# Optimization experiments

Measured on AMD Instinct MI355X. Metric: run time of the kernel, lower is better.

## Reference

```python
import jax, jax.numpy as jnp
import numpy as np

T, B, D_IN, NQ = 256, 2048, 128, 8  # time, batch, input_dim, n_qubits == hidden_dim


def setup_inputs() -> dict:
    key = jax.random.key(0)
    ks = jax.random.split(key, 13)
    s = 1.0 / np.sqrt(D_IN + NQ)
    def lin(ka, kb):
        W = jax.random.uniform(ka, (D_IN + NQ, NQ), jnp.float32, -s, s)
        b = jax.random.uniform(kb, (NQ,), jnp.float32, -s, s)
        return W, b
    Wf, bf = lin(ks[0], ks[1])
    Wi, bi = lin(ks[2], ks[3])
    Wg, bg = lin(ks[4], ks[5])
    Wo, bo = lin(ks[6], ks[7])
    # trainable RX angles per wire for each of the 4 quantum gates
    thf = jax.random.normal(ks[8], (NQ,), jnp.float32) * 0.1
    thi = jax.random.normal(ks[9], (NQ,), jnp.float32) * 0.1
    thg = jax.random.normal(ks[10], (NQ,), jnp.float32) * 0.1
    tho = jax.random.normal(ks[11], (NQ,), jnp.float32) * 0.1
    inputs = jax.random.normal(ks[12], (T, B, D_IN), jnp.float32)
    return {"inputs": inputs, "Wf": Wf, "bf": bf, "Wi": Wi, "bi": bi,
            "Wg": Wg, "bg": bg, "Wo": Wo, "bo": bo,
            "thf": thf, "thi": thi, "thg": thg, "tho": tho}


def _qgate(lin_out, theta):
    # |0..0> -> RX(x_i) encode -> RX(theta_i) trainable -> <PauliZ_i> = cos(x_i + theta_i)
    return jnp.cos(lin_out + theta)


def reference(inputs, Wf, bf, Wi, bi, Wg, bg, Wo, bo, thf, thi, thg, tho):
    Bsz = inputs.shape[1]
    h0 = jnp.zeros((Bsz, NQ), inputs.dtype)
    c0 = jnp.zeros((Bsz, NQ), inputs.dtype)

    def step(carry, x):
        hx, cx = carry
        comb = jnp.concatenate([x, hx], axis=1)  # [B, D_IN+NQ]
        f = jax.nn.sigmoid(_qgate(comb @ Wf + bf, thf))
        i = jax.nn.sigmoid(_qgate(comb @ Wi + bi, thi))
        g = jnp.tanh(_qgate(comb @ Wg + bg, thg))
        o = jax.nn.sigmoid(_qgate(comb @ Wo + bo, tho))
        cx = f * cx + i * g
        hx = o * jnp.tanh(cx)
        return (hx, cx), hx

    (hx, cx), outputs = jax.lax.scan(step, (h0, c0), inputs)
    return outputs, hx, cx
```

## Files before the change

### kernel.cpp

```cpp
#include <hip/hip_runtime.h>

#define T_DIM 256
#define B_DIM 2048
#define D_IN_DIM 128
#define NQ 8
#define ROWS_PER_BLK 64
#define XSTRIDE 129
#define TSTRIDE 33

__global__ __launch_bounds__(256) void qlstm_gemm(
    const float* __restrict__ X,
    const float* __restrict__ Wf, const float* __restrict__ Wi,
    const float* __restrict__ Wg, const float* __restrict__ Wo,
    const float* __restrict__ bf, const float* __restrict__ bi,
    const float* __restrict__ bg, const float* __restrict__ bo,
    const float* __restrict__ thf, const float* __restrict__ thi,
    const float* __restrict__ thg, const float* __restrict__ tho,
    float4* __restrict__ Z)
{
    __shared__ float xs[ROWS_PER_BLK * XSTRIDE];

    const int t = (int)threadIdx.x;
    const int r0 = (int)blockIdx.x * ROWS_PER_BLK;

    const float4* Xg = (const float4*)(X + (size_t)r0 * D_IN_DIM);
#pragma unroll
    for (int i = 0; i < 8; i++) {
        int L = t + i * 256;
        float4 v = Xg[L];
        int row = L >> 5;
        int k4  = L & 31;
        float* d = &xs[row * XSTRIDE + k4 * 4];
        d[0] = v.x; d[1] = v.y; d[2] = v.z; d[3] = v.w;
    }
    __syncthreads();

    const int wid  = __builtin_amdgcn_readfirstlane(t >> 6);
    const int lane = t & 63;

    const float* W  = (wid == 0) ? Wf  : (wid == 1) ? Wi  : (wid == 2) ? Wg  : Wo;
    const float* BB = (wid == 0) ? bf  : (wid == 1) ? bi  : (wid == 2) ? bg  : bo;
    const float* TH = (wid == 0) ? thf : (wid == 1) ? thi : (wid == 2) ? thg : tho;

    float acc[NQ];
#pragma unroll
    for (int q = 0; q < NQ; q++) acc[q] = BB[q] + TH[q];

    const float* xrow = &xs[lane * XSTRIDE];
#pragma unroll 4
    for (int k = 0; k < D_IN_DIM; k++) {
        float xk = xrow[k];
#pragma unroll
        for (int q = 0; q < NQ; q++)
            acc[q] += xk * W[k * NQ + q];
    }

    __syncthreads();
    float* tile = xs;
#pragma unroll
    for (int q = 0; q < NQ; q++)
        tile[lane * TSTRIDE + q * 4 + wid] = acc[q];
    __syncthreads();

    float4* Zblk = Z + (size_t)r0 * NQ;
#pragma unroll
    for (int i = 0; i < 2; i++) {
        int F = t + i * 256;
        int r = F >> 3, q = F & 7;
        const float* s = &tile[r * TSTRIDE + q * 4];
        Zblk[F] = make_float4(s[0], s[1], s[2], s[3]);
    }
}

#define INV_2PI 0.15915494309189535f
#define L2E     1.4426950408889634f

__device__ __forceinline__ float hw_cos(float x) {
    return __builtin_amdgcn_cosf(x * INV_2PI);
}
__device__ __forceinline__ float hw_sig(float x) {
    return __builtin_amdgcn_rcpf(1.0f + __builtin_amdgcn_exp2f(-L2E * x));
}
__device__ __forceinline__ float hw_tanh(float x) {
    return 1.0f - 2.0f * __builtin_amdgcn_rcpf(__builtin_amdgcn_exp2f((2.0f * L2E) * x) + 1.0f);
}

#define BCAST8(x, J) \
    __int_as_float(__builtin_amdgcn_ds_swizzle(__float_as_int(x), ((J) << 5) | 0x18))

#define DOT_TERM(J) { \
    float hj = BCAST8(h, J); \
    accf += hj * whf[J]; acci += hj * whi[J]; \
    accg += hj * whg[J]; acco += hj * who[J]; }

#define LSTM_STEP(zv, outp) { \
    float accf = (zv).x, acci = (zv).y, accg = (zv).z, acco = (zv).w; \
    DOT_TERM(0) DOT_TERM(1) DOT_TERM(2) DOT_TERM(3) \
    DOT_TERM(4) DOT_TERM(5) DOT_TERM(6) DOT_TERM(7) \
    float fg = hw_sig(hw_cos(accf)); \
    float ig = hw_sig(hw_cos(acci)); \
    float gg = hw_tanh(hw_cos(accg)); \
    float og = hw_sig(hw_cos(acco)); \
    c = fg * c + ig * gg; \
    h = og * hw_tanh(c); \
    *(outp) = h; }

__global__ __launch_bounds__(64) void qlstm_recur(
    const float4* __restrict__ Z,
    const float* __restrict__ Wf, const float* __restrict__ Wi,
    const float* __restrict__ Wg, const float* __restrict__ Wo,
    float* __restrict__ out,
    float* __restrict__ state,
    int t0, int ct, int first, int last)
{
    const int tid = (int)blockIdx.x * 64 + (int)threadIdx.x;
    const int q   = tid & 7;

    float whf[8], whi[8], whg[8], who[8];
#pragma unroll
    for (int j = 0; j < 8; j++) {
        whf[j] = Wf[(D_IN_DIM + j) * NQ + q];
        whi[j] = Wi[(D_IN_DIM + j) * NQ + q];
        whg[j] = Wg[(D_IN_DIM + j) * NQ + q];
        who[j] = Wo[(D_IN_DIM + j) * NQ + q];
    }

    float h, c;
    if (first) { h = 0.0f; c = 0.0f; }
    else       { h = state[tid]; c = state[B_DIM * NQ + tid]; }

    const size_t stepsz = (size_t)B_DIM * NQ;
    const float4* Zp = Z + tid;
    float* outp = out + (size_t)t0 * stepsz + tid;

    float4 bufA[8], bufB[8];
#pragma unroll
    for (int s = 0; s < 8; s++) bufA[s] = Zp[(size_t)s * stepsz];

    for (int tb = 0; tb < ct; tb += 16) {
#pragma unroll
        for (int s = 0; s < 8; s++) bufB[s] = Zp[(size_t)(tb + 8 + s) * stepsz];
        __builtin_amdgcn_sched_barrier(0);
#pragma unroll
        for (int s = 0; s < 8; s++) {
            float4 z = bufA[s];
            LSTM_STEP(z, outp)
            outp += stepsz;
        }
        if (tb + 16 < ct) {
#pragma unroll
            for (int s = 0; s < 8; s++) bufA[s] = Zp[(size_t)(tb + 16 + s) * stepsz];
        }
        __builtin_amdgcn_sched_barrier(0);
#pragma unroll
        for (int s = 0; s < 8; s++) {
            float4 z = bufB[s];
            LSTM_STEP(z, outp)
            outp += stepsz;
        }
    }

    if (last) {
        out[(size_t)T_DIM * stepsz + tid] = h;
        out[(size_t)T_DIM * stepsz + stepsz + tid] = c;
    } else {
        state[tid] = h;
        state[B_DIM * NQ + tid] = c;
    }
}

extern "C" void kernel_launch(void* const* d_in, const int* in_sizes, int n_in,
                              void* d_out, int out_size, void* d_ws, size_t ws_size,
                              hipStream_t stream) {
    const float* X   = (const float*)d_in[0];
    const float* Wf  = (const float*)d_in[1];
    const float* bf  = (const float*)d_in[2];
    const float* Wi  = (const float*)d_in[3];
    const float* bi  = (const float*)d_in[4];
    const float* Wg  = (const float*)d_in[5];
    const float* bg  = (const float*)d_in[6];
    const float* Wo  = (const float*)d_in[7];
    const float* bo  = (const float*)d_in[8];
    const float* thf = (const float*)d_in[9];
    const float* thi = (const float*)d_in[10];
    const float* thg = (const float*)d_in[11];
    const float* tho = (const float*)d_in[12];
    float* out = (float*)d_out;

    const size_t state_bytes = (size_t)2 * B_DIM * NQ * sizeof(float);
    float* state = (float*)d_ws;
    float4* Zbuf = (float4*)((char*)d_ws + state_bytes);
    size_t avail = ws_size > state_bytes ? ws_size - state_bytes : 0;
    const size_t z_bytes_per_t = (size_t)B_DIM * NQ * sizeof(float4);
    int maxChunkT = (int)(avail / z_bytes_per_t);
    if (maxChunkT > T_DIM) maxChunkT = T_DIM;
    maxChunkT &= ~15;
    if (maxChunkT < 16) maxChunkT = 16;

    int t0 = 0;
    int first = 1;
    while (t0 < T_DIM) {
        int ct = (T_DIM - t0 < maxChunkT) ? (T_DIM - t0) : maxChunkT;
        int rows = ct * B_DIM;
        qlstm_gemm<<<rows / ROWS_PER_BLK, 256, 0, stream>>>(
            X + (size_t)t0 * B_DIM * D_IN_DIM,
            Wf, Wi, Wg, Wo, bf, bi, bg, bo, thf, thi, thg, tho,
            Zbuf);
        int last = (t0 + ct == T_DIM) ? 1 : 0;
        qlstm_recur<<<(B_DIM * NQ) / 64, 64, 0, stream>>>(
            Zbuf, Wf, Wi, Wg, Wo, out, state, t0, ct, first, last);
        t0 += ct;
        first = 0;
    }
}
```

Measured before the change: 458.0 us.

## Double GEMM rows per thread, XOR-swizzle LDS, split recurrence FMA chains

The input-projection GEMM now handles 128 rows per block, so each thread accumulates two rows and reuses the float4 weight loads for both. The padded LDS stride is replaced by an XOR swizzle to avoid bank conflicts. In the recurrent kernel, each gate's 8-term dot product is split into two independent FMA chains to shorten the serial dependency. Output stores are batched per 8-step group rather than issued inside every step. These changes raise register use and halve the GEMM grid size.

```diff
diff --git a/kernel.cpp b/kernel.cpp
--- a/kernel.cpp
+++ b/kernel.cpp
@@ -4,9 +4,10 @@
 #define B_DIM 2048
 #define D_IN_DIM 128
 #define NQ 8
-#define ROWS_PER_BLK 64
-#define XSTRIDE 129
+#define ROWS_PER_BLK 128
 #define TSTRIDE 33
+
+#define XSIDX(row, k) (((row) << 7) + ((k) ^ ((row) & 31)))
 
 __global__ __launch_bounds__(256) void qlstm_gemm(
     const float* __restrict__ X,
@@ -18,20 +19,22 @@
     const float* __restrict__ thg, const float* __restrict__ tho,
     float4* __restrict__ Z)
 {
-    __shared__ float xs[ROWS_PER_BLK * XSTRIDE];
+    __shared__ float xs[ROWS_PER_BLK * D_IN_DIM];
 
     const int t = (int)threadIdx.x;
     const int r0 = (int)blockIdx.x * ROWS_PER_BLK;
 
     const float4* Xg = (const float4*)(X + (size_t)r0 * D_IN_DIM);
 #pragma unroll
-    for (int i = 0; i < 8; i++) {
+    for (int i = 0; i < 16; i++) {
         int L = t + i * 256;
         float4 v = Xg[L];
         int row = L >> 5;
-        int k4  = L & 31;
-        float* d = &xs[row * XSTRIDE + k4 * 4];
-        d[0] = v.x; d[1] = v.y; d[2] = v.z; d[3] = v.w;
+        int k0  = (L & 31) * 4;
+        xs[XSIDX(row, k0 + 0)] = v.x;
+        xs[XSIDX(row, k0 + 1)] = v.y;
+        xs[XSIDX(row, k0 + 2)] = v.z;
+        xs[XSIDX(row, k0 + 3)] = v.w;
     }
     __syncthreads();
 
@@ -41,30 +44,39 @@
     const float* W  = (wid == 0) ? Wf  : (wid == 1) ? Wi  : (wid == 2) ? Wg  : Wo;
     const float* BB = (wid == 0) ? bf  : (wid == 1) ? bi  : (wid == 2) ? bg  : bo;
     const float* TH = (wid == 0) ? thf : (wid == 1) ? thi : (wid == 2) ? thg : tho;
-
-    float acc[NQ];
-#pragma unroll
-    for (int q = 0; q < NQ; q++) acc[q] = BB[q] + TH[q];
-
-    const float* xrow = &xs[lane * XSTRIDE];
+    const float4* __restrict__ W4 = (const float4*)W;
+
+    float acc0[NQ], acc1[NQ];
+#pragma unroll
+    for (int q = 0; q < NQ; q++) { float b0 = BB[q] + TH[q]; acc0[q] = b0; acc1[q] = b0; }
+
+    const float* xr0 = &xs[(size_t)lane << 7];
+    const float* xr1 = &xs[(size_t)(lane + 64) << 7];
+    const int sw = lane & 31;
 #pragma unroll 4
     for (int k = 0; k < D_IN_DIM; k++) {
-        float xk = xrow[k];
-#pragma unroll
-        for (int q = 0; q < NQ; q++)
-            acc[q] += xk * W[k * NQ + q];
+        float x0 = xr0[k ^ sw];
+        float x1 = xr1[k ^ sw];
+        float4 wa = W4[2 * k];
+        float4 wb = W4[2 * k + 1];
+        acc0[0] += x0 * wa.x; acc0[1] += x0 * wa.y; acc0[2] += x0 * wa.z; acc0[3] += x0 * wa.w;
+        acc0[4] += x0 * wb.x; acc0[5] += x0 * wb.y; acc0[6] += x0 * wb.z; acc0[7] += x0 * wb.w;
+        acc1[0] += x1 * wa.x; acc1[1] += x1 * wa.y; acc1[2] += x1 * wa.z; acc1[3] += x1 * wa.w;
+        acc1[4] += x1 * wb.x; acc1[5] += x1 * wb.y; acc1[6] += x1 * wb.z; acc1[7] += x1 * wb.w;
     }
 
     __syncthreads();
     float* tile = xs;
 #pragma unroll
-    for (int q = 0; q < NQ; q++)
-        tile[lane * TSTRIDE + q * 4 + wid] = acc[q];
+    for (int q = 0; q < NQ; q++) {
+        tile[lane * TSTRIDE + q * 4 + wid] = acc0[q];
+        tile[(lane + 64) * TSTRIDE + q * 4 + wid] = acc1[q];
+    }
     __syncthreads();
 
     float4* Zblk = Z + (size_t)r0 * NQ;
 #pragma unroll
-    for (int i = 0; i < 2; i++) {
+    for (int i = 0; i < 4; i++) {
         int F = t + i * 256;
         int r = F >> 3, q = F & 7;
         const float* s = &tile[r * TSTRIDE + q * 4];
@@ -88,22 +100,32 @@
 #define BCAST8(x, J) \
     __int_as_float(__builtin_amdgcn_ds_swizzle(__float_as_int(x), ((J) << 5) | 0x18))
 
-#define DOT_TERM(J) { \
-    float hj = BCAST8(h, J); \
-    accf += hj * whf[J]; acci += hj * whi[J]; \
-    accg += hj * whg[J]; acco += hj * who[J]; }
-
-#define LSTM_STEP(zv, outp) { \
-    float accf = (zv).x, acci = (zv).y, accg = (zv).z, acco = (zv).w; \
-    DOT_TERM(0) DOT_TERM(1) DOT_TERM(2) DOT_TERM(3) \
-    DOT_TERM(4) DOT_TERM(5) DOT_TERM(6) DOT_TERM(7) \
-    float fg = hw_sig(hw_cos(accf)); \
-    float ig = hw_sig(hw_cos(acci)); \
-    float gg = hw_tanh(hw_cos(accg)); \
-    float og = hw_sig(hw_cos(acco)); \
-    c = fg * c + ig * gg; \
+#define LSTM_STEP_R(zv, hdst) { \
+    float h0 = BCAST8(h, 0), h1 = BCAST8(h, 1), h2 = BCAST8(h, 2), h3 = BCAST8(h, 3); \
+    float h4 = BCAST8(h, 4), h5 = BCAST8(h, 5), h6 = BCAST8(h, 6), h7 = BCAST8(h, 7); \
+    float f0 = fmaf(h0, whf[0], (zv).x), f1 = fmaf(h1, whf[1], 0.0f); \
+    float i0 = fmaf(h0, whi[0], (zv).y), i1 = fmaf(h1, whi[1], 0.0f); \
+    float g0 = fmaf(h0, whg[0], (zv).z), g1 = fmaf(h1, whg[1], 0.0f); \
+    float o0 = fmaf(h0, who[0], (zv).w), o1 = fmaf(h1, who[1], 0.0f); \
+    f0 = fmaf(h2, whf[2], f0); f1 = fmaf(h3, whf[3], f1); \
+    i0 = fmaf(h2, whi[2], i0); i1 = fmaf(h3, whi[3], i1); \
+    g0 = fmaf(h2, whg[2], g0); g1 = fmaf(h3, whg[3], g1); \
+    o0 = fmaf(h2, who[2], o0); o1 = fmaf(h3, who[3], o1); \
+    f0 = fmaf(h4, whf[4], f0); f1 = fmaf(h5, whf[5], f1); \
+    i0 = fmaf(h4, whi[4], i0); i1 = fmaf(h5, whi[5], i1); \
+    g0 = fmaf(h4, whg[4], g0); g1 = fmaf(h5, whg[5], g1); \
+    o0 = fmaf(h4, who[4], o0); o1 = fmaf(h5, who[5], o1); \
+    f0 = fmaf(h6, whf[6], f0); f1 = fmaf(h7, whf[7], f1); \
+    i0 = fmaf(h6, whi[6], i0); i1 = fmaf(h7, whi[7], i1); \
+    g0 = fmaf(h6, whg[6], g0); g1 = fmaf(h7, whg[7], g1); \
+    o0 = fmaf(h6, who[6], o0); o1 = fmaf(h7, who[7], o1); \
+    float fg = hw_sig(hw_cos(f0 + f1)); \
+    float ig = hw_sig(hw_cos(i0 + i1)); \
+    float gg = hw_tanh(hw_cos(g0 + g1)); \
+    float og = hw_sig(hw_cos(o0 + o1)); \
+    c = fmaf(fg, c, ig * gg); \
     h = og * hw_tanh(c); \
-    *(outp) = h; }
+    (hdst) = h; }
 
 __global__ __launch_bounds__(64) void qlstm_recur(
     const float4* __restrict__ Z,
@@ -131,9 +153,10 @@
 
     const size_t stepsz = (size_t)B_DIM * NQ;
     const float4* Zp = Z + tid;
-    float* outp = out + (size_t)t0 * stepsz + tid;
+    float* og_ptr = out + (size_t)t0 * stepsz + tid;
 
     float4 bufA[8], bufB[8];
+    float houtA[8], houtB[8];
 #pragma unroll
     for (int s = 0; s < 8; s++) bufA[s] = Zp[(size_t)s * stepsz];
 
@@ -144,8 +167,7 @@
 #pragma unroll
         for (int s = 0; s < 8; s++) {
             float4 z = bufA[s];
-            LSTM_STEP(z, outp)
-            outp += stepsz;
+            LSTM_STEP_R(z, houtA[s])
         }
         if (tb + 16 < ct) {
 #pragma unroll
@@ -153,11 +175,15 @@
         }
         __builtin_amdgcn_sched_barrier(0);
 #pragma unroll
+        for (int s = 0; s < 8; s++) og_ptr[(size_t)s * stepsz] = houtA[s];
+#pragma unroll
         for (int s = 0; s < 8; s++) {
             float4 z = bufB[s];
-            LSTM_STEP(z, outp)
-            outp += stepsz;
+            LSTM_STEP_R(z, houtB[s])
         }
+#pragma unroll
+        for (int s = 0; s < 8; s++) og_ptr[(size_t)(8 + s) * stepsz] = houtB[s];
+        og_ptr += (size_t)16 * stepsz;
     }
 
     if (last) {
```

After: 479.8 us. +4.8%, slower.
